# Kernel optimization log

Measured on AMD Instinct MI355X. Metric: run time of the kernel, lower is better.

Reference implementation:

```python
import jax, jax.numpy as jnp
import numpy as np

# HalfKA_v2 canonical constants
FT_INPUT_DIM = 45056
FT_OUTPUT_DIM = 1024
PSQT_BUCKETS = 8
LAYER_STACKS = 8
FC0_OUT = 16
L2 = 15
FC1_IN_PAD = 32
FC1_OUT = 32
FC2_IN_PAD = 32
B = 8192
FEATS = 32  # active features per sample


def round_ste(x):
    # forward: round; backward: identity (straight-through)
    return x + jax.lax.stop_gradient(jnp.round(x) - x)


def fake_quant(w, bits):
    qmax = (1 << (bits - 1)) - 1
    return jnp.clip(round_ste(w), -qmax - 1, qmax)


def sparse_sum(w, feats, offsets, nb):
    # EmbeddingBag(mode='sum'): gather rows and segment-sum per sample.
    gathered = w[feats]                               # [total_feats, D]
    n = feats.shape[0]
    sid = jnp.zeros((n,), jnp.int32).at[offsets[1:]].set(1).cumsum()
    return jax.ops.segment_sum(gathered, sid, num_segments=nb)


def setup_inputs() -> dict:
    key = jax.random.key(0)
    ks = jax.random.split(key, 8)
    w_feats = jax.random.randint(ks[0], (B * FEATS,), 0, FT_INPUT_DIM)
    b_feats = jax.random.randint(ks[1], (B * FEATS,), 0, FT_INPUT_DIM)
    offs = jnp.arange(B, dtype=jnp.int32) * FEATS
    stm = jax.random.randint(ks[2], (B,), 0, 2)
    bucket = jax.random.randint(ks[3], (B,), 0, LAYER_STACKS)
    ft_weight = jax.random.normal(ks[4], (FT_INPUT_DIM, FT_OUTPUT_DIM), jnp.float32) * 5.0
    ft_bias = jnp.full((FT_OUTPUT_DIM,), 30.0, jnp.float32)
    psqt_weight = jnp.zeros((FT_INPUT_DIM, PSQT_BUCKETS), jnp.float32)
    fc0_w = jax.random.normal(ks[5], (LAYER_STACKS, FC0_OUT, FT_OUTPUT_DIM), jnp.float32) * 3.0
    fc0_b = jnp.zeros((LAYER_STACKS, FC0_OUT), jnp.float32)
    fc1_w = jax.random.normal(ks[6], (LAYER_STACKS, FC1_OUT, FC1_IN_PAD), jnp.float32) * 3.0
    fc1_b = jnp.zeros((LAYER_STACKS, FC1_OUT), jnp.float32)
    fc2_w = jax.random.normal(ks[7], (LAYER_STACKS, 1, FC2_IN_PAD), jnp.float32) * 3.0
    fc2_b = jnp.zeros((LAYER_STACKS, 1), jnp.float32)
    return dict(w_feats=w_feats, w_offsets=offs, b_feats=b_feats, b_offsets=offs,
                stm=stm, bucket=bucket, ft_weight=ft_weight, ft_bias=ft_bias,
                psqt_weight=psqt_weight, fc0_w=fc0_w, fc0_b=fc0_b,
                fc1_w=fc1_w, fc1_b=fc1_b, fc2_w=fc2_w, fc2_b=fc2_b)


def reference(w_feats, w_offsets, b_feats, b_offsets, stm, bucket,
              ft_weight, ft_bias, psqt_weight,
              fc0_w, fc0_b, fc1_w, fc1_b, fc2_w, fc2_b):
    nb = stm.shape[0]
    ftw = fake_quant(ft_weight, 16)
    ftb = fake_quant(ft_bias, 16)
    psq = fake_quant(psqt_weight, 32)

    acc_w = sparse_sum(ftw, w_feats, w_offsets, nb) + ftb
    acc_b = sparse_sum(ftw, b_feats, b_offsets, nb) + ftb
    psqt_w = sparse_sum(psq, w_feats, w_offsets, nb)
    psqt_b = sparse_sum(psq, b_feats, b_offsets, nb)

    stm_f = stm.astype(ft_weight.dtype)[:, None]
    acc_stm = acc_w * (1 - stm_f) + acc_b * stm_f
    acc_opp = acc_b * (1 - stm_f) + acc_w * stm_f

    H = FT_OUTPUT_DIM // 2

    def pairwise(a):
        return jnp.clip(a[:, :H], 0.0, 127.0) * jnp.clip(a[:, H:], 0.0, 127.0) / 128.0

    ft = jnp.concatenate([pairwise(acc_stm), pairwise(acc_opp)], axis=-1)  # [B, 1024]

    fc0w = fake_quant(fc0_w, 8); fc0b = fake_quant(fc0_b, 32)
    fc1w = fake_quant(fc1_w, 8); fc1b = fake_quant(fc1_b, 32)
    fc2w = fake_quant(fc2_w, 8); fc2b = fake_quant(fc2_b, 32)

    bsel3 = bucket[:, None, None]
    # fc0: compute all 8 tiny stacks, then select per-sample bucket (equivalent to mask routing)
    o0_all = jnp.einsum('bf,sof->bso', ft, fc0w) + fc0b[None]      # [B, S, 16]
    o0 = jnp.take_along_axis(o0_all, bsel3, axis=1)[:, 0]           # [B, 16]

    sqr = jnp.clip(o0[:, :L2] ** 2 / float(1 << 19), 0.0, 127.0)
    rel = jnp.clip(o0[:, :L2] / float(1 << 6), 0.0, 127.0)
    slab = jnp.concatenate([sqr, rel, jnp.zeros((nb, FC1_IN_PAD - 2 * L2), ft.dtype)], axis=-1)

    o1_all = jnp.einsum('bi,soi->bso', slab, fc1w) + fc1b[None]     # [B, S, 32]
    o1 = jnp.take_along_axis(o1_all, bsel3, axis=1)[:, 0]
    ac1 = jnp.clip(o1 / float(1 << 6), 0.0, 127.0)

    o2_all = jnp.einsum('bi,soi->bso', ac1, fc2w) + fc2b[None]      # [B, S, 1]
    scalar = jnp.take_along_axis(o2_all, bsel3, axis=1)[:, 0]       # [B, 1]

    skip = o0[:, 15:16] * (9600.0 / 8128.0)
    positional = scalar + skip

    psqt_stm = psqt_w * (1 - stm_f) + psqt_b * stm_f
    psqt_opp = psqt_b * (1 - stm_f) + psqt_w * stm_f
    bsel = bucket[:, None]
    psqt_v = (jnp.take_along_axis(psqt_stm, bsel, axis=1)
              - jnp.take_along_axis(psqt_opp, bsel, axis=1)) / 2.0

    return ((psqt_v + positional)[:, 0]) / 16.0
```

## Files before the change

kernel.cpp:

```cpp
#include <hip/hip_runtime.h>


#define NFEATS 32
#define TBL_BYTES  (45056u * 1024u)
#define TBL_N4     11534336
#define TBL_G8     (TBL_N4 / 8)
#define W0_CHUNKS  (8 * 16 * 64)
#define FC1_N4     2048
#define FC2_N4     64
#define BIAS_CHUNKS 64
#define OFF_W0   ((size_t)TBL_BYTES)
#define OFF_W1   (OFF_W0 + (size_t)8 * 16 * 1024 * 4)
#define OFF_W2   (OFF_W1 + (size_t)8 * 32 * 32 * 4)
#define OFF_BI   (OFF_W2 + (size_t)8 * 32 * 4)
#define WS_NEED  (OFF_BI + 2048)

typedef short v2s __attribute__((ext_vector_type(2)));

__device__ __forceinline__ float q16f(float x) {
    float r = rintf(x);
    return fminf(fmaxf(r, -32768.f), 32767.f);
}
__device__ __forceinline__ float q8f(float x) {
    float r = rintf(x);
    return fminf(fmaxf(r, -128.f), 127.f);
}
__device__ __forceinline__ float4 q8f4(float4 v) {
    return make_float4(q8f(v.x), q8f(v.y), q8f(v.z), q8f(v.w));
}
__device__ __forceinline__ float clip127(float x) {
    return fminf(fmaxf(x, 0.f), 127.f);
}
__device__ __forceinline__ v2s sx_even(int p) {
    union { int i; v2s s; } u; u.i = p << 8; u.s = u.s >> 8; return u.s;
}
__device__ __forceinline__ v2s sx_odd(int p) {
    union { int i; v2s s; } u; u.i = p; u.s = u.s >> 8; return u.s;
}
__device__ __forceinline__ void acc8(v2s a[8], int4 p) {
    a[0] += sx_even(p.x); a[1] += sx_odd(p.x);
    a[2] += sx_even(p.y); a[3] += sx_odd(p.y);
    a[4] += sx_even(p.z); a[5] += sx_odd(p.z);
    a[6] += sx_even(p.w); a[7] += sx_odd(p.w);
}
__device__ __forceinline__ v2s clip_pk(v2s v) {
    v2s r;
    r.x = v.x < 0 ? 0 : (v.x > 127 ? (short)127 : v.x);
    r.y = v.y < 0 ? 0 : (v.y > 127 ? (short)127 : v.y);
    return r;
}
__device__ __forceinline__ int v2s_as_int(v2s v) {
    union { v2s s; int i; } u; u.s = v; return u.i;
}
__device__ __forceinline__ v2s int_as_v2s(int v) {
    union { int i; v2s s; } u; u.i = v; return u.s;
}

__device__ __forceinline__ int pack4i8(float4 v) {
    const int a = (int)rintf(fminf(fmaxf(v.x, -127.f), 127.f));
    const int b = (int)rintf(fminf(fmaxf(v.y, -127.f), 127.f));
    const int c = (int)rintf(fminf(fmaxf(v.z, -127.f), 127.f));
    const int d = (int)rintf(fminf(fmaxf(v.w, -127.f), 127.f));
    return (a & 0xff) | ((b & 0xff) << 8) | ((c & 0xff) << 16) | (d << 24);
}

__global__ __launch_bounds__(256) void cvt_v4(
    const float4* __restrict__ tbl, const float* __restrict__ fc0,
    const float4* __restrict__ fc1, const float4* __restrict__ fc2,
    const float* __restrict__ ft_bias, char* __restrict__ ws)
{
    const int i = blockIdx.x * 256 + threadIdx.x;
    if (i < TBL_G8) {
        const float4* p = tbl + (size_t)i * 8;
        int4 a, b;
        a.x = pack4i8(p[0]); a.y = pack4i8(p[1]);
        a.z = pack4i8(p[2]); a.w = pack4i8(p[3]);
        b.x = pack4i8(p[4]); b.y = pack4i8(p[5]);
        b.z = pack4i8(p[6]); b.w = pack4i8(p[7]);
        int4* o = (int4*)ws;
        o[2 * (size_t)i]     = a;
        o[2 * (size_t)i + 1] = b;
        return;
    }
    int j = i - TBL_G8;
    if (j < W0_CHUNKS) {
        const float4* s = (const float4*)(fc0 + (size_t)j * 16);
        const float4 a = q8f4(s[0]), b = q8f4(s[1]),
                     c = q8f4(s[2]), d = q8f4(s[3]);
        float4* o = (float4*)(ws + OFF_W0 + (size_t)j * 64);
        o[0] = make_float4(a.x, a.z, a.y, a.w);
        o[1] = make_float4(b.x, b.z, b.y, b.w);
        o[2] = make_float4(c.x, c.z, c.y, c.w);
        o[3] = make_float4(d.x, d.z, d.y, d.w);
        return;
    }
    j -= W0_CHUNKS;
    if (j < FC1_N4) { ((float4*)(ws + OFF_W1))[j] = q8f4(fc1[j]); return; }
    j -= FC1_N4;
    if (j < FC2_N4) { ((float4*)(ws + OFF_W2))[j] = q8f4(fc2[j]); return; }
    j -= FC2_N4;
    if (j < BIAS_CHUNKS) {
        const float* s = ft_bias + j * 16;
        short tmp[16];
        #pragma unroll
        for (int g = 0; g < 4; ++g) {
            tmp[4 * g + 0] = (short)q16f(s[4 * g + 0]);
            tmp[4 * g + 1] = (short)q16f(s[4 * g + 2]);
            tmp[4 * g + 2] = (short)q16f(s[4 * g + 1]);
            tmp[4 * g + 3] = (short)q16f(s[4 * g + 3]);
        }
        int4* o = (int4*)(ws + OFF_BI + (size_t)j * 32);
        o[0] = *(const int4*)&tmp[0];
        o[1] = *(const int4*)&tmp[8];
    }
}

__global__ __launch_bounds__(256, 4) void nnue_v4(
    const int* __restrict__ w_feats, const int* __restrict__ w_offsets,
    const int* __restrict__ b_feats, const int* __restrict__ b_offsets,
    const int* __restrict__ stm_arr, const int* __restrict__ bucket_arr,
    const char* __restrict__ tbl,   const float* __restrict__ w0q,
    const float* __restrict__ w1q,  const float* __restrict__ w2q,
    const char* __restrict__ biasI, const float* __restrict__ psqt_weight,
    const float* __restrict__ fc0_b, const float* __restrict__ fc1_b,
    const float* __restrict__ fc2_b,
    float* __restrict__ out, int n_wf, int n_bf, int nb)
{
    const int t = threadIdx.x;
    const int l = t & 63;
    const int wv = t >> 6;
    const int p = blockIdx.x * 4 + wv;
    if (p >= nb) return;

    const int fs = w_offsets[p];
    const int fe = (p + 1 < nb) ? w_offsets[p + 1] : n_wf;
    const int gs = b_offsets[p];
    const int ge = (p + 1 < nb) ? b_offsets[p + 1] : n_bf;
    const int cw = min(fe - fs, NFEATS);
    const int cb = min(ge - gs, NFEATS);

    const int k32 = l & 31;
    int myidx = 0;
    if (l < 32) { if (k32 < cw) myidx = w_feats[fs + k32]; }
    else        { if (k32 < cb) myidx = b_feats[gs + k32]; }

    const int stm = stm_arr[p];
    const int bk  = bucket_arr[p];

    v2s aw[8] = {{0,0},{0,0},{0,0},{0,0},{0,0},{0,0},{0,0},{0,0}};
    v2s ab[8] = {{0,0},{0,0},{0,0},{0,0},{0,0},{0,0},{0,0},{0,0}};

    if (cw == NFEATS && cb == NFEATS) {
        #pragma unroll
        for (int k = 0; k < NFEATS; ++k) {
            const int rw = __builtin_amdgcn_readlane(myidx, k);
            const int rb = __builtin_amdgcn_readlane(myidx, 32 + k);
            const int4 pw = ((const int4*)(tbl + ((size_t)rw << 10)))[l];
            const int4 pb = ((const int4*)(tbl + ((size_t)rb << 10)))[l];
            acc8(aw, pw);
            acc8(ab, pb);
        }
    } else {
        #pragma unroll
        for (int k = 0; k < NFEATS; ++k) {
            if (k < cw) {
                const int rw = __builtin_amdgcn_readlane(myidx, k);
                acc8(aw, ((const int4*)(tbl + ((size_t)rw << 10)))[l]);
            }
            if (k < cb) {
                const int rb = __builtin_amdgcn_readlane(myidx, 32 + k);
                acc8(ab, ((const int4*)(tbl + ((size_t)rb << 10)))[l]);
            }
        }
    }

    {
        union { int4 q[2]; v2s s[8]; } bb;
        bb.q[0] = ((const int4*)biasI)[2 * l];
        bb.q[1] = ((const int4*)biasI)[2 * l + 1];
        #pragma unroll
        for (int i = 0; i < 8; ++i) { aw[i] += bb.s[i]; ab[i] += bb.s[i]; }
    }

    float ftf[16];
    {
        const bool low = (l < 32);
        #pragma unroll
        for (int i = 0; i < 8; ++i) {
            const v2s sv = stm ? ab[i] : aw[i];
            const v2s ov = stm ? aw[i] : ab[i];
            const v2s own  = low ? sv : ov;
            const int send = v2s_as_int(low ? ov : sv);
            const v2s rcv  = int_as_v2s(__shfl_xor(send, 32));
            const v2s a = clip_pk(own);
            const v2s b = clip_pk(rcv);
            ftf[2 * i]     = (float)(a.x * b.x) * 0.0078125f;
            ftf[2 * i + 1] = (float)(a.y * b.y) * 0.0078125f;
        }
    }

    float s0[16];
    {
        const float4* w0p = (const float4*)(w0q + (size_t)bk * 16 * 1024);
        #pragma unroll
        for (int o = 0; o < 16; ++o) {
            const float4* wr = w0p + o * 256 + l * 4;
            const float4 A = wr[0], B = wr[1], C = wr[2], D = wr[3];
            s0[o] = ftf[0]  * A.x + ftf[1]  * A.y + ftf[2]  * A.z + ftf[3]  * A.w
                  + ftf[4]  * B.x + ftf[5]  * B.y + ftf[6]  * B.z + ftf[7]  * B.w
                  + ftf[8]  * C.x + ftf[9]  * C.y + ftf[10] * C.z + ftf[11] * C.w
                  + ftf[12] * D.x + ftf[13] * D.y + ftf[14] * D.z + ftf[15] * D.w;
        }
        #pragma unroll
        for (int o = 0; o < 16; ++o) {
            float v = s0[o];
            v += __shfl_xor(v, 32);
            v += __shfl_xor(v, 16);
            v += __shfl_xor(v,  8);
            v += __shfl_xor(v,  4);
            v += __shfl_xor(v,  2);
            v += __shfl_xor(v,  1);
            s0[o] = v;
        }
    }

    float o0v[16];
    {
        const float* b0 = fc0_b + bk * 16;
        #pragma unroll
        for (int o = 0; o < 16; ++o) o0v[o] = s0[o] + rintf(b0[o]);
    }
    float sqr[15], rel[15];
    #pragma unroll
    for (int i = 0; i < 15; ++i) {
        sqr[i] = clip127(o0v[i] * o0v[i] * (1.f / 524288.f));
        rel[i] = clip127(o0v[i] * 0.015625f);
    }

    float ac1v;
    {
        const int j = l & 31;
        const float4* w1r = (const float4*)(w1q + ((size_t)bk * 32 + j) * 32);
        const float4 W0 = w1r[0], W1 = w1r[1], W2 = w1r[2], W3 = w1r[3];
        const float4 W4 = w1r[4], W5 = w1r[5], W6 = w1r[6], W7 = w1r[7];
        float a1 = rintf(fc1_b[bk * 32 + j]);
        a1 += sqr[0]  * W0.x + sqr[1]  * W0.y + sqr[2]  * W0.z + sqr[3]  * W0.w
            + sqr[4]  * W1.x + sqr[5]  * W1.y + sqr[6]  * W1.z + sqr[7]  * W1.w
            + sqr[8]  * W2.x + sqr[9]  * W2.y + sqr[10] * W2.z + sqr[11] * W2.w
            + sqr[12] * W3.x + sqr[13] * W3.y + sqr[14] * W3.z + rel[0]  * W3.w
            + rel[1]  * W4.x + rel[2]  * W4.y + rel[3]  * W4.z + rel[4]  * W4.w
            + rel[5]  * W5.x + rel[6]  * W5.y + rel[7]  * W5.z + rel[8]  * W5.w
            + rel[9]  * W6.x + rel[10] * W6.y + rel[11] * W6.z + rel[12] * W6.w
            + rel[13] * W7.x + rel[14] * W7.y;
        ac1v = clip127(a1 * 0.015625f);
    }

    float pr2;
    {
        const float wv2 = w2q[bk * 32 + (l & 31)];
        pr2 = (l < 32) ? ac1v * wv2 : 0.f;
        pr2 += __shfl_xor(pr2, 32);
        pr2 += __shfl_xor(pr2, 16);
        pr2 += __shfl_xor(pr2,  8);
        pr2 += __shfl_xor(pr2,  4);
        pr2 += __shfl_xor(pr2,  2);
        pr2 += __shfl_xor(pr2,  1);
    }

    float pv = 0.f;
    {
        const bool valid = (l < 32) ? (k32 < cw) : (k32 < cb);
        if (valid) pv = rintf(psqt_weight[myidx * 8 + bk]);
        pv += __shfl_xor(pv,  1);
        pv += __shfl_xor(pv,  2);
        pv += __shfl_xor(pv,  4);
        pv += __shfl_xor(pv,  8);
        pv += __shfl_xor(pv, 16);
    }
    const float cross = __shfl_xor(pv, 32);

    if (l == 0) {
        const float o2   = pr2 + rintf(fc2_b[bk]);
        const float skip = o0v[15] * (float)(9600.0 / 8128.0);
        const float ps   = stm ? cross : pv;
        const float po   = stm ? pv : cross;
        out[p] = (0.5f * (ps - po) + o2 + skip) * 0.0625f;
    }
}

__global__ __launch_bounds__(256) void nnue_fb(
    const int* __restrict__ w_feats, const int* __restrict__ w_offsets,
    const int* __restrict__ b_feats, const int* __restrict__ b_offsets,
    const int* __restrict__ stm_arr, const int* __restrict__ bucket_arr,
    const float* __restrict__ ft_weight, const float* __restrict__ ft_bias,
    const float* __restrict__ psqt_weight,
    const float* __restrict__ fc0_w, const float* __restrict__ fc0_b,
    const float* __restrict__ fc1_w, const float* __restrict__ fc1_b,
    const float* __restrict__ fc2_w, const float* __restrict__ fc2_b,
    float* __restrict__ out, int n_wf, int n_bf, int nb)
{
    const int b = blockIdx.x;
    const int t = threadIdx.x;
    const int l = t & 63;
    const int w = t >> 6;

    __shared__ int s_fw[NFEATS], s_fb[NFEATS];
    __shared__ __align__(16) float s_acc[2][1024];
    __shared__ __align__(16) float s_ft[1024];
    __shared__ float s_o0[16];
    __shared__ float s_slab[32];
    __shared__ float s_ac1[32];
    __shared__ float s_psqt[2];

    const int ws = w_offsets[b];
    const int we = (b + 1 < nb) ? w_offsets[b + 1] : n_wf;
    const int bs = b_offsets[b];
    const int be = (b + 1 < nb) ? b_offsets[b + 1] : n_bf;
    const int cw = min(we - ws, NFEATS);
    const int cb = min(be - bs, NFEATS);

    if (t < NFEATS) s_fw[t] = (t < cw) ? w_feats[ws + t] : 0;
    else if (t < 2 * NFEATS) {
        const int k = t - NFEATS;
        s_fb[k] = (k < cb) ? b_feats[bs + k] : 0;
    }
    __syncthreads();

    const int stm = stm_arr[b];
    const int bk  = bucket_arr[b];

    if (t < 64) {
        const int side = t >> 5;
        const int k = t & 31;
        const int cnt = side ? cb : cw;
        float v = 0.f;
        if (k < cnt) v = rintf(psqt_weight[(side ? s_fb[k] : s_fw[k]) * 8 + bk]);
        v += __shfl_down(v, 16, 32); v += __shfl_down(v, 8, 32);
        v += __shfl_down(v, 4, 32);  v += __shfl_down(v, 2, 32);
        v += __shfl_down(v, 1, 32);
        if (k == 0) s_psqt[side] = v;
    }

    const float4* ftw4 = reinterpret_cast<const float4*>(ft_weight);
    float4 aw = make_float4(0, 0, 0, 0), ab = make_float4(0, 0, 0, 0);
    for (int k = 0; k < cw; ++k) {
        const float4 v = ftw4[s_fw[k] * 256 + t];
        aw.x += rintf(v.x); aw.y += rintf(v.y);
        aw.z += rintf(v.z); aw.w += rintf(v.w);
    }
    for (int k = 0; k < cb; ++k) {
        const float4 u = ftw4[s_fb[k] * 256 + t];
        ab.x += rintf(u.x); ab.y += rintf(u.y);
        ab.z += rintf(u.z); ab.w += rintf(u.w);
    }
    const float4 bv = reinterpret_cast<const float4*>(ft_bias)[t];
    aw.x += q16f(bv.x); aw.y += q16f(bv.y); aw.z += q16f(bv.z); aw.w += q16f(bv.w);
    ab.x += q16f(bv.x); ab.y += q16f(bv.y); ab.z += q16f(bv.z); ab.w += q16f(bv.w);
    reinterpret_cast<float4*>(&s_acc[0][4 * t])[0] = aw;
    reinterpret_cast<float4*>(&s_acc[1][4 * t])[0] = ab;
    __syncthreads();

    {
        float4 lo, hi;
        if (t < 128) {
            const float* sp = s_acc[stm];
            lo = ((const float4*)sp)[t]; hi = ((const float4*)sp)[t + 128];
        } else {
            const float* sp = s_acc[1 - stm];
            lo = ((const float4*)sp)[t - 128]; hi = ((const float4*)sp)[t];
        }
        float4 r;
        r.x = clip127(lo.x) * clip127(hi.x) * 0.0078125f;
        r.y = clip127(lo.y) * clip127(hi.y) * 0.0078125f;
        r.z = clip127(lo.z) * clip127(hi.z) * 0.0078125f;
        r.w = clip127(lo.w) * clip127(hi.w) * 0.0078125f;
        ((float4*)s_ft)[t] = r;
    }
    __syncthreads();

    {
        const float4* ftf4 = (const float4*)s_ft;
        const float4 f0 = ftf4[l], f1 = ftf4[l + 64],
                     f2 = ftf4[l + 128], f3 = ftf4[l + 192];
        #pragma unroll
        for (int o = 0; o < 4; ++o) {
            const int orow = 4 * w + o;
            const float4* wr = (const float4*)fc0_w + ((size_t)bk * 16 + orow) * 256;
            const float4 w0 = q8f4(wr[l]), w1 = q8f4(wr[l + 64]),
                         w2 = q8f4(wr[l + 128]), w3 = q8f4(wr[l + 192]);
            float acc = f0.x * w0.x + f0.y * w0.y + f0.z * w0.z + f0.w * w0.w
                      + f1.x * w1.x + f1.y * w1.y + f1.z * w1.z + f1.w * w1.w
                      + f2.x * w2.x + f2.y * w2.y + f2.z * w2.z + f2.w * w2.w
                      + f3.x * w3.x + f3.y * w3.y + f3.z * w3.z + f3.w * w3.w;
            acc += __shfl_down(acc, 32); acc += __shfl_down(acc, 16);
            acc += __shfl_down(acc, 8);  acc += __shfl_down(acc, 4);
            acc += __shfl_down(acc, 2);  acc += __shfl_down(acc, 1);
            if (l == 0) s_o0[orow] = acc + rintf(fc0_b[bk * 16 + orow]);
        }
    }
    __syncthreads();

    if (t < 32) {
        float v;
        if (t < 15)      v = clip127(s_o0[t] * s_o0[t] * (1.f / 524288.f));
        else if (t < 30) v = clip127(s_o0[t - 15] * 0.015625f);
        else             v = 0.f;
        s_slab[t] = v;
    }
    __syncthreads();

    if (t < 32) {
        const float* w1 = fc1_w + (size_t)bk * 32 * 32 + t * 32;
        float acc = rintf(fc1_b[bk * 32 + t]);
        #pragma unroll
        for (int i = 0; i < 32; ++i) acc += s_slab[i] * q8f(w1[i]);
        s_ac1[t] = clip127(acc * 0.015625f);
    }
    __syncthreads();

    if (t == 0) {
        const float* w2 = fc2_w + (size_t)bk * 32;
        float acc = rintf(fc2_b[bk]);
        #pragma unroll
        for (int i = 0; i < 32; ++i) acc += s_ac1[i] * q8f(w2[i]);
        const float skip = s_o0[15] * (float)(9600.0 / 8128.0);
        const float ps = stm ? s_psqt[1] : s_psqt[0];
        const float po = stm ? s_psqt[0] : s_psqt[1];
        out[b] = (0.5f * (ps - po) + acc + skip) * 0.0625f;
    }
}

extern "C" void kernel_launch(void* const* d_in, const int* in_sizes, int n_in,
                              void* d_out, int out_size, void* d_ws, size_t ws_size,
                              hipStream_t stream) {
    const int*   w_feats   = (const int*)d_in[0];
    const int*   w_offsets = (const int*)d_in[1];
    const int*   b_feats   = (const int*)d_in[2];
    const int*   b_offsets = (const int*)d_in[3];
    const int*   stm       = (const int*)d_in[4];
    const int*   bucket    = (const int*)d_in[5];
    const float* ft_weight = (const float*)d_in[6];
    const float* ft_bias   = (const float*)d_in[7];
    const float* psqt_w    = (const float*)d_in[8];
    const float* fc0_w     = (const float*)d_in[9];
    const float* fc0_b     = (const float*)d_in[10];
    const float* fc1_w     = (const float*)d_in[11];
    const float* fc1_b     = (const float*)d_in[12];
    const float* fc2_w     = (const float*)d_in[13];
    const float* fc2_b     = (const float*)d_in[14];
    float*       out       = (float*)d_out;

    const int nb   = in_sizes[4];
    const int n_wf = in_sizes[0];
    const int n_bf = in_sizes[2];

    if (ws_size >= WS_NEED) {
        const int nthreads = TBL_G8 + W0_CHUNKS + FC1_N4 + FC2_N4 + BIAS_CHUNKS;
        cvt_v4<<<(nthreads + 255) / 256, 256, 0, stream>>>(
            (const float4*)ft_weight, fc0_w, (const float4*)fc1_w,
            (const float4*)fc2_w, ft_bias, (char*)d_ws);

        const char*  tbl  = (const char*)d_ws;
        const float* w0q  = (const float*)((char*)d_ws + OFF_W0);
        const float* w1q  = (const float*)((char*)d_ws + OFF_W1);
        const float* w2q  = (const float*)((char*)d_ws + OFF_W2);
        const char*  bi   = (const char*)d_ws + OFF_BI;

        nnue_v4<<<(nb + 3) / 4, 256, 0, stream>>>(
            w_feats, w_offsets, b_feats, b_offsets, stm, bucket,
            tbl, w0q, w1q, w2q, bi, psqt_w, fc0_b, fc1_b, fc2_b,
            out, n_wf, n_bf, nb);
    } else {
        nnue_fb<<<nb, 256, 0, stream>>>(
            w_feats, w_offsets, b_feats, b_offsets, stm, bucket,
            ft_weight, ft_bias, psqt_w,
            fc0_w, fc0_b, fc1_w, fc1_b, fc2_w, fc2_b,
            out, n_wf, n_bf, nb);
    }
}
```

Measured before the change: 382.4 us.

## Restructure NNUE kernel to one sample per 128-thread block with perspective-split waves

The main kernel now gives each sample its own 128-thread block. Each wave gathers one perspective's feature rows, loading two 8-byte halves per lane instead of 16-byte quads, and the two waves combine their fc0 partials through shared memory and a transposing shuffle reduction. The conversion kernel is simplified to a straight int8 pack per float4 with no reordering of fc0, and the bias is read and quantized inline. This is meant to improve gather parallelism and to drop the bias preprocessing, at the cost of per-block shared-memory syncs, smaller loads and more blocks.

```diff
diff --git a/kernel.cpp b/kernel.cpp
--- a/kernel.cpp
+++ b/kernel.cpp
@@ -4,16 +4,13 @@
 #define NFEATS 32
 #define TBL_BYTES  (45056u * 1024u)
 #define TBL_N4     11534336
-#define TBL_G8     (TBL_N4 / 8)
-#define W0_CHUNKS  (8 * 16 * 64)
+#define FC0_N4     32768
 #define FC1_N4     2048
 #define FC2_N4     64
-#define BIAS_CHUNKS 64
 #define OFF_W0   ((size_t)TBL_BYTES)
-#define OFF_W1   (OFF_W0 + (size_t)8 * 16 * 1024 * 4)
-#define OFF_W2   (OFF_W1 + (size_t)8 * 32 * 32 * 4)
-#define OFF_BI   (OFF_W2 + (size_t)8 * 32 * 4)
-#define WS_NEED  (OFF_BI + 2048)
+#define OFF_W1   (OFF_W0 + (size_t)FC0_N4 * 16)
+#define OFF_W2   (OFF_W1 + (size_t)FC1_N4 * 16)
+#define WS_NEED  (OFF_W2 + (size_t)FC2_N4 * 16)
 
 typedef short v2s __attribute__((ext_vector_type(2)));
 
@@ -36,24 +33,6 @@
 }
 __device__ __forceinline__ v2s sx_odd(int p) {
     union { int i; v2s s; } u; u.i = p; u.s = u.s >> 8; return u.s;
-}
-__device__ __forceinline__ void acc8(v2s a[8], int4 p) {
-    a[0] += sx_even(p.x); a[1] += sx_odd(p.x);
-    a[2] += sx_even(p.y); a[3] += sx_odd(p.y);
-    a[4] += sx_even(p.z); a[5] += sx_odd(p.z);
-    a[6] += sx_even(p.w); a[7] += sx_odd(p.w);
-}
-__device__ __forceinline__ v2s clip_pk(v2s v) {
-    v2s r;
-    r.x = v.x < 0 ? 0 : (v.x > 127 ? (short)127 : v.x);
-    r.y = v.y < 0 ? 0 : (v.y > 127 ? (short)127 : v.y);
-    return r;
-}
-__device__ __forceinline__ int v2s_as_int(v2s v) {
-    union { v2s s; int i; } u; u.s = v; return u.i;
-}
-__device__ __forceinline__ v2s int_as_v2s(int v) {
-    union { int i; v2s s; } u; u.i = v; return u.s;
 }
 
 __device__ __forceinline__ int pack4i8(float4 v) {
@@ -64,227 +43,226 @@
     return (a & 0xff) | ((b & 0xff) << 8) | ((c & 0xff) << 16) | (d << 24);
 }
 
-__global__ __launch_bounds__(256) void cvt_v4(
-    const float4* __restrict__ tbl, const float* __restrict__ fc0,
+__global__ __launch_bounds__(256) void cvt_v5(
+    const float4* __restrict__ tbl, const float4* __restrict__ fc0,
     const float4* __restrict__ fc1, const float4* __restrict__ fc2,
-    const float* __restrict__ ft_bias, char* __restrict__ ws)
+    char* __restrict__ ws)
 {
     const int i = blockIdx.x * 256 + threadIdx.x;
-    if (i < TBL_G8) {
-        const float4* p = tbl + (size_t)i * 8;
-        int4 a, b;
-        a.x = pack4i8(p[0]); a.y = pack4i8(p[1]);
-        a.z = pack4i8(p[2]); a.w = pack4i8(p[3]);
-        b.x = pack4i8(p[4]); b.y = pack4i8(p[5]);
-        b.z = pack4i8(p[6]); b.w = pack4i8(p[7]);
-        int4* o = (int4*)ws;
-        o[2 * (size_t)i]     = a;
-        o[2 * (size_t)i + 1] = b;
+    if (i < TBL_N4) {
+        ((int*)ws)[i] = pack4i8(tbl[i]);
         return;
     }
-    int j = i - TBL_G8;
-    if (j < W0_CHUNKS) {
-        const float4* s = (const float4*)(fc0 + (size_t)j * 16);
-        const float4 a = q8f4(s[0]), b = q8f4(s[1]),
-                     c = q8f4(s[2]), d = q8f4(s[3]);
-        float4* o = (float4*)(ws + OFF_W0 + (size_t)j * 64);
-        o[0] = make_float4(a.x, a.z, a.y, a.w);
-        o[1] = make_float4(b.x, b.z, b.y, b.w);
-        o[2] = make_float4(c.x, c.z, c.y, c.w);
-        o[3] = make_float4(d.x, d.z, d.y, d.w);
-        return;
-    }
-    j -= W0_CHUNKS;
+    int j = i - TBL_N4;
+    if (j < FC0_N4) { ((float4*)(ws + OFF_W0))[j] = q8f4(fc0[j]); return; }
+    j -= FC0_N4;
     if (j < FC1_N4) { ((float4*)(ws + OFF_W1))[j] = q8f4(fc1[j]); return; }
     j -= FC1_N4;
-    if (j < FC2_N4) { ((float4*)(ws + OFF_W2))[j] = q8f4(fc2[j]); return; }
-    j -= FC2_N4;
-    if (j < BIAS_CHUNKS) {
-        const float* s = ft_bias + j * 16;
-        short tmp[16];
-        #pragma unroll
-        for (int g = 0; g < 4; ++g) {
-            tmp[4 * g + 0] = (short)q16f(s[4 * g + 0]);
-            tmp[4 * g + 1] = (short)q16f(s[4 * g + 2]);
-            tmp[4 * g + 2] = (short)q16f(s[4 * g + 1]);
-            tmp[4 * g + 3] = (short)q16f(s[4 * g + 3]);
-        }
-        int4* o = (int4*)(ws + OFF_BI + (size_t)j * 32);
-        o[0] = *(const int4*)&tmp[0];
-        o[1] = *(const int4*)&tmp[8];
-    }
-}
-
-__global__ __launch_bounds__(256, 4) void nnue_v4(
+    if (j < FC2_N4) { ((float4*)(ws + OFF_W2))[j] = q8f4(fc2[j]); }
+}
+
+__global__ __launch_bounds__(128) void nnue_v5(
     const int* __restrict__ w_feats, const int* __restrict__ w_offsets,
     const int* __restrict__ b_feats, const int* __restrict__ b_offsets,
     const int* __restrict__ stm_arr, const int* __restrict__ bucket_arr,
     const char* __restrict__ tbl,   const float* __restrict__ w0q,
     const float* __restrict__ w1q,  const float* __restrict__ w2q,
-    const char* __restrict__ biasI, const float* __restrict__ psqt_weight,
+    const float* __restrict__ ft_bias, const float* __restrict__ psqt_weight,
     const float* __restrict__ fc0_b, const float* __restrict__ fc1_b,
     const float* __restrict__ fc2_b,
     float* __restrict__ out, int n_wf, int n_bf, int nb)
 {
+    const int b = blockIdx.x;
     const int t = threadIdx.x;
     const int l = t & 63;
-    const int wv = t >> 6;
-    const int p = blockIdx.x * 4 + wv;
-    if (p >= nb) return;
-
-    const int fs = w_offsets[p];
-    const int fe = (p + 1 < nb) ? w_offsets[p + 1] : n_wf;
-    const int gs = b_offsets[p];
-    const int ge = (p + 1 < nb) ? b_offsets[p + 1] : n_bf;
+    const int grpB = t >> 6;
+
+    __shared__ int   s_fw[NFEATS], s_fb[NFEATS];
+    __shared__ float s_red[2][16];
+    __shared__ float s_psqt[2];
+
+    const int fs = w_offsets[b];
+    const int fe = (b + 1 < nb) ? w_offsets[b + 1] : n_wf;
+    const int gs = b_offsets[b];
+    const int ge = (b + 1 < nb) ? b_offsets[b + 1] : n_bf;
     const int cw = min(fe - fs, NFEATS);
     const int cb = min(ge - gs, NFEATS);
 
-    const int k32 = l & 31;
-    int myidx = 0;
-    if (l < 32) { if (k32 < cw) myidx = w_feats[fs + k32]; }
-    else        { if (k32 < cb) myidx = b_feats[gs + k32]; }
-
-    const int stm = stm_arr[p];
-    const int bk  = bucket_arr[p];
-
-    v2s aw[8] = {{0,0},{0,0},{0,0},{0,0},{0,0},{0,0},{0,0},{0,0}};
-    v2s ab[8] = {{0,0},{0,0},{0,0},{0,0},{0,0},{0,0},{0,0},{0,0}};
-
-    if (cw == NFEATS && cb == NFEATS) {
-        #pragma unroll
+    if (t < 32)                    s_fw[t] = (t < cw) ? w_feats[fs + t] : 0;
+    else if (t >= 64 && t < 96) {
+        const int k = t - 64;
+        s_fb[k] = (k < cb) ? b_feats[gs + k] : 0;
+    }
+    __syncthreads();
+
+    const int stm = stm_arr[b];
+    const int bk  = bucket_arr[b];
+
+    if (l < 32) {
+        const int cnt = grpB ? cb : cw;
+        float v = 0.f;
+        if (l < cnt) {
+            const int f = grpB ? s_fb[l] : s_fw[l];
+            v = rintf(psqt_weight[f * 8 + bk]);
+        }
+        v += __shfl_down(v, 16, 32);
+        v += __shfl_down(v,  8, 32);
+        v += __shfl_down(v,  4, 32);
+        v += __shfl_down(v,  2, 32);
+        v += __shfl_down(v,  1, 32);
+        if (l == 0) s_psqt[grpB] = v;
+    }
+
+    const int* rows = (grpB ^ stm) ? s_fb : s_fw;
+    const int  cnt  = (grpB ^ stm) ? cb : cw;
+    const char* cp  = tbl + 8 * l;
+
+    v2s le0 = {0,0}, lo0 = {0,0}, le1 = {0,0}, lo1 = {0,0};
+    v2s he0 = {0,0}, ho0 = {0,0}, he1 = {0,0}, ho1 = {0,0};
+
+    if (cnt == NFEATS) {
+        #pragma unroll 8
         for (int k = 0; k < NFEATS; ++k) {
-            const int rw = __builtin_amdgcn_readlane(myidx, k);
-            const int rb = __builtin_amdgcn_readlane(myidx, 32 + k);
-            const int4 pw = ((const int4*)(tbl + ((size_t)rw << 10)))[l];
-            const int4 pb = ((const int4*)(tbl + ((size_t)rb << 10)))[l];
-            acc8(aw, pw);
-            acc8(ab, pb);
+            const char* rp = cp + ((size_t)rows[k] << 10);
+            const int2 plo = *(const int2*)rp;
+            const int2 phi = *(const int2*)(rp + 512);
+            le0 += sx_even(plo.x); lo0 += sx_odd(plo.x);
+            le1 += sx_even(plo.y); lo1 += sx_odd(plo.y);
+            he0 += sx_even(phi.x); ho0 += sx_odd(phi.x);
+            he1 += sx_even(phi.y); ho1 += sx_odd(phi.y);
         }
     } else {
-        #pragma unroll
-        for (int k = 0; k < NFEATS; ++k) {
-            if (k < cw) {
-                const int rw = __builtin_amdgcn_readlane(myidx, k);
-                acc8(aw, ((const int4*)(tbl + ((size_t)rw << 10)))[l]);
-            }
-            if (k < cb) {
-                const int rb = __builtin_amdgcn_readlane(myidx, 32 + k);
-                acc8(ab, ((const int4*)(tbl + ((size_t)rb << 10)))[l]);
-            }
-        }
-    }
-
+        for (int k = 0; k < cnt; ++k) {
+            const char* rp = cp + ((size_t)rows[k] << 10);
+            const int2 plo = *(const int2*)rp;
+            const int2 phi = *(const int2*)(rp + 512);
+            le0 += sx_even(plo.x); lo0 += sx_odd(plo.x);
+            le1 += sx_even(plo.y); lo1 += sx_odd(plo.y);
+            he0 += sx_even(phi.x); ho0 += sx_odd(phi.x);
+            he1 += sx_even(phi.y); ho1 += sx_odd(phi.y);
+        }
+    }
+
+    float ftf[8];
     {
-        union { int4 q[2]; v2s s[8]; } bb;
-        bb.q[0] = ((const int4*)biasI)[2 * l];
-        bb.q[1] = ((const int4*)biasI)[2 * l + 1];
-        #pragma unroll
-        for (int i = 0; i < 8; ++i) { aw[i] += bb.s[i]; ab[i] += bb.s[i]; }
-    }
-
-    float ftf[16];
+        const float4 bA = ((const float4*)(ft_bias + 8 * l))[0];
+        const float4 bB = ((const float4*)(ft_bias + 8 * l))[1];
+        const float4 cA = ((const float4*)(ft_bias + 8 * l + 512))[0];
+        const float4 cB = ((const float4*)(ft_bias + 8 * l + 512))[1];
+        float lo_f[8] = {
+            (float)le0.x + q16f(bA.x), (float)lo0.x + q16f(bA.y),
+            (float)le0.y + q16f(bA.z), (float)lo0.y + q16f(bA.w),
+            (float)le1.x + q16f(bB.x), (float)lo1.x + q16f(bB.y),
+            (float)le1.y + q16f(bB.z), (float)lo1.y + q16f(bB.w) };
+        float hi_f[8] = {
+            (float)he0.x + q16f(cA.x), (float)ho0.x + q16f(cA.y),
+            (float)he0.y + q16f(cA.z), (float)ho0.y + q16f(cA.w),
+            (float)he1.x + q16f(cB.x), (float)ho1.x + q16f(cB.y),
+            (float)he1.y + q16f(cB.z), (float)ho1.y + q16f(cB.w) };
+        #pragma unroll
+        for (int j = 0; j < 8; ++j)
+            ftf[j] = clip127(lo_f[j]) * clip127(hi_f[j]) * 0.0078125f;
+    }
+
+    float v[16];
     {
-        const bool low = (l < 32);
-        #pragma unroll
-        for (int i = 0; i < 8; ++i) {
-            const v2s sv = stm ? ab[i] : aw[i];
-            const v2s ov = stm ? aw[i] : ab[i];
-            const v2s own  = low ? sv : ov;
-            const int send = v2s_as_int(low ? ov : sv);
-            const v2s rcv  = int_as_v2s(__shfl_xor(send, 32));
-            const v2s a = clip_pk(own);
-            const v2s b = clip_pk(rcv);
-            ftf[2 * i]     = (float)(a.x * b.x) * 0.0078125f;
-            ftf[2 * i + 1] = (float)(a.y * b.y) * 0.0078125f;
-        }
-    }
-
-    float s0[16];
+        const int wcol = grpB * 512 + 8 * l;
+        const float* w0r = w0q + (size_t)bk * 16 * 1024 + wcol;
+        #pragma unroll
+        for (int o = 0; o < 16; ++o) {
+            const float4 A = ((const float4*)(w0r + o * 1024))[0];
+            const float4 B = ((const float4*)(w0r + o * 1024))[1];
+            v[o] = ftf[0] * A.x + ftf[1] * A.y + ftf[2] * A.z + ftf[3] * A.w
+                 + ftf[4] * B.x + ftf[5] * B.y + ftf[6] * B.z + ftf[7] * B.w;
+        }
+    }
+
     {
-        const float4* w0p = (const float4*)(w0q + (size_t)bk * 16 * 1024);
-        #pragma unroll
-        for (int o = 0; o < 16; ++o) {
-            const float4* wr = w0p + o * 256 + l * 4;
-            const float4 A = wr[0], B = wr[1], C = wr[2], D = wr[3];
-            s0[o] = ftf[0]  * A.x + ftf[1]  * A.y + ftf[2]  * A.z + ftf[3]  * A.w
-                  + ftf[4]  * B.x + ftf[5]  * B.y + ftf[6]  * B.z + ftf[7]  * B.w
-                  + ftf[8]  * C.x + ftf[9]  * C.y + ftf[10] * C.z + ftf[11] * C.w
-                  + ftf[12] * D.x + ftf[13] * D.y + ftf[14] * D.z + ftf[15] * D.w;
-        }
-        #pragma unroll
-        for (int o = 0; o < 16; ++o) {
-            float v = s0[o];
-            v += __shfl_xor(v, 32);
-            v += __shfl_xor(v, 16);
-            v += __shfl_xor(v,  8);
-            v += __shfl_xor(v,  4);
-            v += __shfl_xor(v,  2);
-            v += __shfl_xor(v,  1);
-            s0[o] = v;
-        }
-    }
-
-    float o0v[16];
-    {
-        const float* b0 = fc0_b + bk * 16;
-        #pragma unroll
-        for (int o = 0; o < 16; ++o) o0v[o] = s0[o] + rintf(b0[o]);
-    }
-    float sqr[15], rel[15];
-    #pragma unroll
-    for (int i = 0; i < 15; ++i) {
-        sqr[i] = clip127(o0v[i] * o0v[i] * (1.f / 524288.f));
-        rel[i] = clip127(o0v[i] * 0.015625f);
-    }
-
-    float ac1v;
-    {
-        const int j = l & 31;
-        const float4* w1r = (const float4*)(w1q + ((size_t)bk * 32 + j) * 32);
-        const float4 W0 = w1r[0], W1 = w1r[1], W2 = w1r[2], W3 = w1r[3];
-        const float4 W4 = w1r[4], W5 = w1r[5], W6 = w1r[6], W7 = w1r[7];
-        float a1 = rintf(fc1_b[bk * 32 + j]);
-        a1 += sqr[0]  * W0.x + sqr[1]  * W0.y + sqr[2]  * W0.z + sqr[3]  * W0.w
-            + sqr[4]  * W1.x + sqr[5]  * W1.y + sqr[6]  * W1.z + sqr[7]  * W1.w
-            + sqr[8]  * W2.x + sqr[9]  * W2.y + sqr[10] * W2.z + sqr[11] * W2.w
-            + sqr[12] * W3.x + sqr[13] * W3.y + sqr[14] * W3.z + rel[0]  * W3.w
-            + rel[1]  * W4.x + rel[2]  * W4.y + rel[3]  * W4.z + rel[4]  * W4.w
-            + rel[5]  * W5.x + rel[6]  * W5.y + rel[7]  * W5.z + rel[8]  * W5.w
-            + rel[9]  * W6.x + rel[10] * W6.y + rel[11] * W6.z + rel[12] * W6.w
-            + rel[13] * W7.x + rel[14] * W7.y;
-        ac1v = clip127(a1 * 0.015625f);
-    }
-
-    float pr2;
-    {
-        const float wv2 = w2q[bk * 32 + (l & 31)];
-        pr2 = (l < 32) ? ac1v * wv2 : 0.f;
+        #pragma unroll
+        for (int j = 0; j < 8; ++j) {
+            const bool up = (l & 1);
+            const float send = up ? v[j] : v[j + 8];
+            const float r = __shfl_xor(send, 1);
+            v[j] = (up ? v[j + 8] : v[j]) + r;
+        }
+        #pragma unroll
+        for (int j = 0; j < 4; ++j) {
+            const bool up = (l & 2);
+            const float send = up ? v[j] : v[j + 4];
+            const float r = __shfl_xor(send, 2);
+            v[j] = (up ? v[j + 4] : v[j]) + r;
+        }
+        #pragma unroll
+        for (int j = 0; j < 2; ++j) {
+            const bool up = (l & 4);
+            const float send = up ? v[j] : v[j + 2];
+            const float r = __shfl_xor(send, 4);
+            v[j] = (up ? v[j + 2] : v[j]) + r;
+        }
+        {
+            const bool up = (l & 8);
+            const float send = up ? v[0] : v[1];
+            const float r = __shfl_xor(send, 8);
+            v[0] = (up ? v[1] : v[0]) + r;
+        }
+        v[0] += __shfl_xor(v[0], 16);
+        v[0] += __shfl_xor(v[0], 32);
+        if (l < 16) {
+            const int o = ((l & 1) << 3) | ((l & 2) << 1)
+                        | ((l & 4) >> 1) | ((l & 8) >> 3);
+            s_red[grpB][o] = v[0];
+        }
+    }
+    __syncthreads();
+
+    if (t < 64) {
+        float o0v[16];
+        {
+            const float* b0 = fc0_b + bk * 16;
+            #pragma unroll
+            for (int o = 0; o < 16; ++o)
+                o0v[o] = s_red[0][o] + s_red[1][o] + rintf(b0[o]);
+        }
+        float sqr[15], rel[15];
+        #pragma unroll
+        for (int i = 0; i < 15; ++i) {
+            sqr[i] = clip127(o0v[i] * o0v[i] * (1.f / 524288.f));
+            rel[i] = clip127(o0v[i] * 0.015625f);
+        }
+
+        float ac1v;
+        {
+            const int j = l & 31;
+            const float4* w1r = (const float4*)(w1q + ((size_t)bk * 32 + j) * 32);
+            const float4 W0 = w1r[0], W1 = w1r[1], W2 = w1r[2], W3 = w1r[3];
+            const float4 W4 = w1r[4], W5 = w1r[5], W6 = w1r[6], W7 = w1r[7];
+            float a1 = rintf(fc1_b[bk * 32 + j]);
+            a1 += sqr[0]  * W0.x + sqr[1]  * W0.y + sqr[2]  * W0.z + sqr[3]  * W0.w
+                + sqr[4]  * W1.x + sqr[5]  * W1.y + sqr[6]  * W1.z + sqr[7]  * W1.w
+                + sqr[8]  * W2.x + sqr[9]  * W2.y + sqr[10] * W2.z + sqr[11] * W2.w
+                + sqr[12] * W3.x + sqr[13] * W3.y + sqr[14] * W3.z + rel[0]  * W3.w
+                + rel[1]  * W4.x + rel[2]  * W4.y + rel[3]  * W4.z + rel[4]  * W4.w
+                + rel[5]  * W5.x + rel[6]  * W5.y + rel[7]  * W5.z + rel[8]  * W5.w
+                + rel[9]  * W6.x + rel[10] * W6.y + rel[11] * W6.z + rel[12] * W6.w
+                + rel[13] * W7.x + rel[14] * W7.y;
+            ac1v = clip127(a1 * 0.015625f);
+        }
+
+        float pr2 = (l < 32) ? ac1v * w2q[bk * 32 + (l & 31)] : 0.f;
         pr2 += __shfl_xor(pr2, 32);
         pr2 += __shfl_xor(pr2, 16);
         pr2 += __shfl_xor(pr2,  8);
         pr2 += __shfl_xor(pr2,  4);
         pr2 += __shfl_xor(pr2,  2);
         pr2 += __shfl_xor(pr2,  1);
-    }
-
-    float pv = 0.f;
-    {
-        const bool valid = (l < 32) ? (k32 < cw) : (k32 < cb);
-        if (valid) pv = rintf(psqt_weight[myidx * 8 + bk]);
-        pv += __shfl_xor(pv,  1);
-        pv += __shfl_xor(pv,  2);
-        pv += __shfl_xor(pv,  4);
-        pv += __shfl_xor(pv,  8);
-        pv += __shfl_xor(pv, 16);
-    }
-    const float cross = __shfl_xor(pv, 32);
-
-    if (l == 0) {
-        const float o2   = pr2 + rintf(fc2_b[bk]);
-        const float skip = o0v[15] * (float)(9600.0 / 8128.0);
-        const float ps   = stm ? cross : pv;
-        const float po   = stm ? pv : cross;
-        out[p] = (0.5f * (ps - po) + o2 + skip) * 0.0625f;
+
+        if (l == 0) {
+            const float o2   = pr2 + rintf(fc2_b[bk]);
+            const float skip = o0v[15] * (float)(9600.0 / 8128.0);
+            const float ps   = stm ? s_psqt[1] : s_psqt[0];
+            const float po   = stm ? s_psqt[0] : s_psqt[1];
+            out[b] = (0.5f * (ps - po) + o2 + skip) * 0.0625f;
+        }
     }
 }
 
@@ -455,20 +433,19 @@
     const int n_bf = in_sizes[2];
 
     if (ws_size >= WS_NEED) {
-        const int nthreads = TBL_G8 + W0_CHUNKS + FC1_N4 + FC2_N4 + BIAS_CHUNKS;
-        cvt_v4<<<(nthreads + 255) / 256, 256, 0, stream>>>(
-            (const float4*)ft_weight, fc0_w, (const float4*)fc1_w,
-            (const float4*)fc2_w, ft_bias, (char*)d_ws);
-
-        const char*  tbl  = (const char*)d_ws;
-        const float* w0q  = (const float*)((char*)d_ws + OFF_W0);
-        const float* w1q  = (const float*)((char*)d_ws + OFF_W1);
-        const float* w2q  = (const float*)((char*)d_ws + OFF_W2);
-        const char*  bi   = (const char*)d_ws + OFF_BI;
-
-        nnue_v4<<<(nb + 3) / 4, 256, 0, stream>>>(
+        const int nthreads = TBL_N4 + FC0_N4 + FC1_N4 + FC2_N4;
+        cvt_v5<<<(nthreads + 255) / 256, 256, 0, stream>>>(
+            (const float4*)ft_weight, (const float4*)fc0_w,
+            (const float4*)fc1_w, (const float4*)fc2_w, (char*)d_ws);
+
+        const char*  tbl = (const char*)d_ws;
+        const float* w0q = (const float*)((char*)d_ws + OFF_W0);
+        const float* w1q = (const float*)((char*)d_ws + OFF_W1);
+        const float* w2q = (const float*)((char*)d_ws + OFF_W2);
+
+        nnue_v5<<<nb, 128, 0, stream>>>(
             w_feats, w_offsets, b_feats, b_offsets, stm, bucket,
-            tbl, w0q, w1q, w2q, bi, psqt_w, fc0_b, fc1_b, fc2_b,
+            tbl, w0q, w1q, w2q, ft_bias, psqt_w, fc0_b, fc1_b, fc2_b,
             out, n_wf, n_bf, nb);
     } else {
         nnue_fb<<<nb, 256, 0, stream>>>(
```

After: 359.4 us. 1.06x faster.
